# Kernel tuning notes

Measured on AMD Instinct MI355X. Metric: run time of the kernel, lower is better.

Reference implementation:

```python
import jax, jax.numpy as jnp
import numpy as np

EPS = 1e-5
BN_GAMMA = 1.0
BN_BETA = 1e-4  # per torch init: BN weight=1, bias=0.0001


def bn(h):
    # BatchNorm1d in training mode: biased batch variance
    mu = h.mean(axis=0)
    var = h.var(axis=0)
    return (h - mu) * (BN_GAMMA / jnp.sqrt(var + EPS)) + BN_BETA


def gcn_conv(h, W, b, row, col, n, edge_weight=None):
    # PyG-style GCNConv: linear -> add self loops (w=1) -> sym deg norm -> scatter-sum
    h = h @ W
    e = row.shape[0]
    ew = jnp.ones((e,), h.dtype) if edge_weight is None else edge_weight
    loop = jnp.arange(n, dtype=row.dtype)
    r = jnp.concatenate([row, loop])
    c = jnp.concatenate([col, loop])
    w = jnp.concatenate([ew, jnp.ones((n,), h.dtype)])
    deg = jax.ops.segment_sum(w, r, num_segments=n)
    dinv = jnp.where(deg > 0, jax.lax.rsqrt(deg + jnp.where(deg > 0, 0.0, 1.0)), 0.0)
    norm = dinv[r] * w * dinv[c]  # [E+N]
    msg = h[r] * norm[:, None]    # gather + per-edge scale
    out = jax.ops.segment_sum(msg, c, num_segments=n)  # scatter-aggregate
    return out + b


def readout(h, W1, b1, W2, b2):
    h = bn(h) @ W1 + b1
    h = bn(jax.nn.relu(h)) @ W2 + b2
    return jax.nn.log_softmax(h, axis=-1)


def setup_inputs() -> dict:
    key = jax.random.key(0)
    ks = jax.random.split(key, 12)
    N, E, F, H, C = 50000, 800000, 128, 128, 10
    s = 0.05
    return {
        "x": jax.random.normal(ks[0], (N, F), jnp.float32),
        "edge_index": jax.random.randint(ks[1], (2, E), 0, N, jnp.int32),
        "perm": jax.random.permutation(ks[2], N).astype(jnp.int32),
        "W_feat": jax.random.normal(ks[3], (F, H), jnp.float32) * s,
        "b_feat": jnp.zeros((H,), jnp.float32),
        "W_convs": jax.random.normal(ks[4], (3, H, H), jnp.float32) * s,
        "b_convs": jnp.zeros((3, H), jnp.float32),
        "W_ea": jax.random.normal(ks[5], (2 * H, 2), jnp.float32) * s,
        "b_ea": jnp.zeros((2,), jnp.float32),
        "W_na": jax.random.normal(ks[6], (H, 2), jnp.float32) * s,
        "b_na": jnp.zeros((2,), jnp.float32),
        "W_ctx": jax.random.normal(ks[7], (H, H), jnp.float32) * s,
        "b_ctx": jnp.zeros((H,), jnp.float32),
        "W_obj": jax.random.normal(ks[8], (H, H), jnp.float32) * s,
        "b_obj": jnp.zeros((H,), jnp.float32),
        "W_fc1": jax.random.normal(ks[9], (3, H, H), jnp.float32) * s,  # c,o,co
        "b_fc1": jnp.zeros((3, H), jnp.float32),
        "W_fc2": jax.random.normal(ks[10], (3, H, C), jnp.float32) * s,
        "b_fc2": jnp.zeros((3, C), jnp.float32),
    }


def reference(x, edge_index, perm, W_feat, b_feat, W_convs, b_convs, W_ea, b_ea,
              W_na, b_na, W_ctx, b_ctx, W_obj, b_obj, W_fc1, b_fc1, W_fc2, b_fc2):
    n = x.shape[0]
    row, col = edge_index[0], edge_index[1]
    h = bn(x)
    h = jax.nn.relu(h @ W_feat + b_feat)  # conv_feat has gfn=True -> pure linear
    for i in range(3):
        h = jax.nn.relu(gcn_conv(bn(h), W_convs[i], b_convs[i], row, col, n))
    edge_rep = jnp.concatenate([h[row], h[col]], axis=-1)  # [E, 2H]
    edge_att = jax.nn.softmax(edge_rep @ W_ea + b_ea, axis=-1)
    node_att = jax.nn.softmax(h @ W_na + b_na, axis=-1)
    xc = node_att[:, 0:1] * h
    xo = node_att[:, 1:2] * h
    xc = jax.nn.relu(gcn_conv(bn(xc), W_ctx, b_ctx, row, col, n, edge_att[:, 0]))
    xo = jax.nn.relu(gcn_conv(bn(xo), W_obj, b_obj, row, col, n, edge_att[:, 1]))
    xc_logis = readout(xc, W_fc1[0], b_fc1[0], W_fc2[0], b_fc2[0])
    xo_logis = readout(xo, W_fc1[1], b_fc1[1], W_fc2[1], b_fc2[1])
    xco_logis = readout(xc[perm] + xo, W_fc1[2], b_fc1[2], W_fc2[2], b_fc2[2])
    return (xc_logis, xo_logis, xco_logis)
```

## Files before the change

kernel.cpp:

```cpp
#include <hip/hip_runtime.h>
#include <math.h>

#define H 128
#define NCLS 10
#define EPS 1e-5f
#define BN_BETA 1e-4f
#define CS_BLOCKS 256

typedef unsigned short u16;
typedef unsigned int u32;
typedef __attribute__((ext_vector_type(8))) short short8;
typedef __attribute__((ext_vector_type(4))) float floatx4;

__device__ inline float bflo(u32 u) { union { u32 i; float f; } a; a.i = u << 16; return a.f; }
__device__ inline float bfhi(u32 u) { union { u32 i; float f; } a; a.i = u & 0xffff0000u; return a.f; }
__device__ inline u16 f2bf(float f) {
  union { float f; u32 i; } v; v.f = f;
  return (u16)((v.i + 0x7fff + ((v.i >> 16) & 1)) >> 16);
}
__device__ inline u32 pack2(float a, float b) { return (u32)f2bf(a) | ((u32)f2bf(b) << 16); }

__device__ inline void reduce_partials(const float* __restrict__ P, int nb, int stride,
                                       int off0, int f, float* su_out, float* sq_out) {
  float su[8] = {0, 0, 0, 0, 0, 0, 0, 0}, sq[8] = {0, 0, 0, 0, 0, 0, 0, 0};
  int b = 0;
  for (; b + 8 <= nb; b += 8) {
#pragma unroll
    for (int u = 0; u < 8; u++) {
      const float* p = P + (size_t)(b + u) * stride + off0;
      su[u] += p[f];
      sq[u] += p[128 + f];
    }
  }
  for (; b < nb; b++) {
    const float* p = P + (size_t)b * stride + off0;
    su[0] += p[f];
    sq[0] += p[128 + f];
  }
  *su_out = ((su[0] + su[1]) + (su[2] + su[3])) + ((su[4] + su[5]) + (su[6] + su[7]));
  *sq_out = ((sq[0] + sq[1]) + (sq[2] + sq[3])) + ((sq[4] + sq[5]) + (sq[6] + sq[7]));
}

__global__ __launch_bounds__(256) void xstats_kernel(
    const float* __restrict__ x, int n4, float* __restrict__ stp) {
  int tid = threadIdx.x;
  int lane = tid & 63, wave = tid >> 6;
  float s[4] = {0, 0, 0, 0}, q[4] = {0, 0, 0, 0};
  int step = gridDim.x * 256;
  for (int i = blockIdx.x * 256 + tid; i < n4; i += step) {
    float4 v = ((const float4*)x)[i];
    s[0] += v.x; q[0] += v.x * v.x; s[1] += v.y; q[1] += v.y * v.y;
    s[2] += v.z; q[2] += v.z * v.z; s[3] += v.w; q[3] += v.w * v.w;
  }
#pragma unroll
  for (int k = 0; k < 4; k++) { s[k] += __shfl_xor(s[k], 32); q[k] += __shfl_xor(q[k], 32); }
  __shared__ float sm[4][256];
  int col = (lane & 31) * 4;
  if (lane < 32) {
#pragma unroll
    for (int k = 0; k < 4; k++) { sm[wave][col + k] = s[k]; sm[wave][128 + col + k] = q[k]; }
  }
  __syncthreads();
  stp[(size_t)blockIdx.x * 256 + tid] = sm[0][tid] + sm[1][tid] + sm[2][tid] + sm[3][tid];
}

__global__ __launch_bounds__(256) void colstats_kernel(
    const u16* __restrict__ X, int N, float* __restrict__ stp) {
  int tid = threadIdx.x;
  int li = tid & 15, rg = tid >> 4;
  int wave = tid >> 6, lane = tid & 63;
  const uint4* T = (const uint4*)X;
  float s[8] = {0, 0, 0, 0, 0, 0, 0, 0}, q[8] = {0, 0, 0, 0, 0, 0, 0, 0};
  for (int r = blockIdx.x * 16 + rg; r < N; r += CS_BLOCKS * 16) {
    uint4 u = T[(size_t)r * 16 + li];
    float f[8] = {bflo(u.x), bfhi(u.x), bflo(u.y), bfhi(u.y),
                  bflo(u.z), bfhi(u.z), bflo(u.w), bfhi(u.w)};
#pragma unroll
    for (int j = 0; j < 8; j++) { s[j] += f[j]; q[j] += f[j] * f[j]; }
  }
#pragma unroll
  for (int j = 0; j < 8; j++) {
    s[j] += __shfl_xor(s[j], 16); s[j] += __shfl_xor(s[j], 32);
    q[j] += __shfl_xor(q[j], 16); q[j] += __shfl_xor(q[j], 32);
  }
  __shared__ float sm[4][256];
  if ((lane & 48) == 0) {
#pragma unroll
    for (int j = 0; j < 8; j++) {
      sm[wave][li * 8 + j] = s[j];
      sm[wave][128 + li * 8 + j] = q[j];
    }
  }
  __syncthreads();
  stp[(size_t)blockIdx.x * 256 + tid] = sm[0][tid] + sm[1][tid] + sm[2][tid] + sm[3][tid];
}

__device__ inline void fold_body(const float* P, int nb, int stride, int off0,
                                 const float* W, const float* bias,
                                 float invN, int k, u16* Wt, float* cf) {
  int f = threadIdx.x;
  float su, sq;
  reduce_partials(P, nb, stride, off0, f, &su, &sq);
  float mu = su * invN;
  float var = sq * invN - mu * mu;
  float s = 1.0f / sqrtf(fmaxf(var, 0.f) + EPS);
  float w = W[(size_t)f * H + k];
  Wt[(size_t)k * H + f] = f2bf(s * w);
  __shared__ float red[H];
  red[f] = (BN_BETA - mu * s) * w;
  __syncthreads();
  for (int o = 64; o > 0; o >>= 1) {
    if (f < o) red[f] += red[f + o];
    __syncthreads();
  }
  if (f == 0) cf[k] = red[0] + (bias ? bias[k] : 0.f);
}

__global__ __launch_bounds__(128) void fold_kernel(
    const float* P, int nb, const float* W, const float* bias, float invN,
    u16* Wt, float* cf) {
  fold_body(P, nb, 256, 0, W, bias, invN, blockIdx.x, Wt, cf);
}

__global__ __launch_bounds__(128) void fold2_kernel(
    const float* P, int nb, const float* W0, const float* W1, float invN,
    u16* Wt2, float* cf2) {
  int j = blockIdx.x >> 7, k = blockIdx.x & 127;
  fold_body(P, nb, 512, j * 256, j ? W1 : W0, nullptr, invN, k,
            Wt2 + (size_t)j * H * H, cf2 + j * H);
}

__global__ __launch_bounds__(128) void fold3_kernel(
    const float* PC, int nbC, const float* PO, int nbO, const float* PCO, int nbCO,
    const float* W_fc1, const float* b_fc1, float invN, u16* Wt3, float* cf3) {
  int j = blockIdx.x >> 7, k = blockIdx.x & 127;
  const float* P = (j == 0) ? PC : (j == 1) ? PO : PCO;
  int nb = (j == 0) ? nbC : (j == 1) ? nbO : nbCO;
  fold_body(P, nb, 256, 0, W_fc1 + (size_t)j * H * H, b_fc1 + j * H, invN, k,
            Wt3 + (size_t)j * H * H, cf3 + j * H);
}

__global__ __launch_bounds__(128) void fold10x3_kernel(
    const float* stpZ, int nb, const float* W_fc2, const float* b_fc2, float invN,
    float* W2f, float* c2f) {
  int j = blockIdx.x / NCLS, k = blockIdx.x % NCLS;
  const float* P = stpZ + (size_t)j * nb * 256;
  int f = threadIdx.x;
  float su, sq;
  reduce_partials(P, nb, 256, 0, f, &su, &sq);
  float mu = su * invN;
  float var = sq * invN - mu * mu;
  float s = 1.0f / sqrtf(fmaxf(var, 0.f) + EPS);
  float w = W_fc2[(size_t)j * H * NCLS + (size_t)f * NCLS + k];
  W2f[(size_t)j * H * NCLS + (size_t)f * NCLS + k] = s * w;
  __shared__ float red[H];
  red[f] = (BN_BETA - mu * s) * w;
  __syncthreads();
  for (int o = 64; o > 0; o >>= 1) {
    if (f < o) red[f] += red[f + o];
    __syncthreads();
  }
  if (f == 0) c2f[j * 16 + k] = red[0] + b_fc2[j * NCLS + k];
}

__device__ inline void gemm_core(const u16* A, const float* Afp, const u16* Bt,
                                 const float* cf, const float* b2, const float* sumw,
                                 u16* C, int N, int relu, int blk, float* stp) {
  int tid = threadIdx.x;
  int wave = tid >> 6, lane = tid & 63;
  int l15 = lane & 15, quad = lane >> 4;
  int row0 = (blk * 4 + wave) * 16;
  if (row0 >= N && !stp) return;
  int arow = row0 + l15;
  short8 a[4];
  short8 z8 = {0, 0, 0, 0, 0, 0, 0, 0};
  if (Afp) {
#pragma unroll
    for (int k4 = 0; k4 < 4; k4++) {
      if (arow < N) {
        const float* p = Afp + (size_t)arow * H + k4 * 32 + quad * 8;
        float4 f0 = *(const float4*)p;
        float4 f1 = *(const float4*)(p + 4);
        union { short8 s8; u32 u[4]; } cv;
        cv.u[0] = pack2(f0.x, f0.y); cv.u[1] = pack2(f0.z, f0.w);
        cv.u[2] = pack2(f1.x, f1.y); cv.u[3] = pack2(f1.z, f1.w);
        a[k4] = cv.s8;
      } else a[k4] = z8;
    }
  } else {
#pragma unroll
    for (int k4 = 0; k4 < 4; k4++)
      a[k4] = (arow < N) ? *(const short8*)(A + (size_t)arow * H + k4 * 32 + quad * 8) : z8;
  }
  float srow[4];
  if (sumw) {
#pragma unroll
    for (int r = 0; r < 4; r++) {
      int row = row0 + quad * 4 + r;
      srow[r] = (row < N) ? sumw[row] : 0.f;
    }
  }
  float ps[8], pq[8];
#pragma unroll
  for (int nt = 0; nt < 8; nt++) {
    floatx4 acc = {0.f, 0.f, 0.f, 0.f};
    const u16* bp = Bt + (size_t)(nt * 16 + l15) * H + quad * 8;
#pragma unroll
    for (int k4 = 0; k4 < 4; k4++) {
      short8 b = *(const short8*)(bp + k4 * 32);
      acc = __builtin_amdgcn_mfma_f32_16x16x32_bf16(a[k4], b, acc, 0, 0, 0);
    }
    int col = nt * 16 + l15;
    float base = cf[col];
    float bb = b2 ? b2[col] : 0.f;
    float s_ = 0.f, q_ = 0.f;
#pragma unroll
    for (int r = 0; r < 4; r++) {
      int row = row0 + quad * 4 + r;
      if (row < N) {
        float v = acc[r] + (sumw ? srow[r] * base + bb : base);
        if (relu) v = fmaxf(v, 0.f);
        s_ += v; q_ += v * v;
        C[(size_t)row * H + col] = f2bf(v);
      }
    }
    ps[nt] = s_; pq[nt] = q_;
  }
  if (stp) {
    __shared__ float sred[4][256];
#pragma unroll
    for (int nt = 0; nt < 8; nt++) {
      ps[nt] += __shfl_xor(ps[nt], 16); ps[nt] += __shfl_xor(ps[nt], 32);
      pq[nt] += __shfl_xor(pq[nt], 16); pq[nt] += __shfl_xor(pq[nt], 32);
    }
    if (quad == 0) {
#pragma unroll
      for (int nt = 0; nt < 8; nt++) {
        sred[wave][nt * 16 + l15] = ps[nt];
        sred[wave][128 + nt * 16 + l15] = pq[nt];
      }
    }
    __syncthreads();
    stp[(size_t)blk * 256 + tid] =
        sred[0][tid] + sred[1][tid] + sred[2][tid] + sred[3][tid];
  }
}

__global__ __launch_bounds__(256) void gemm_kernel(
    const u16* A, const u16* Bt, const float* cf, u16* C, int N, int relu) {
  gemm_core(A, nullptr, Bt, cf, nullptr, nullptr, C, N, relu, blockIdx.x, nullptr);
}

__global__ __launch_bounds__(256) void gemm_x_kernel(
    const float* x, const u16* Bt, const float* cf, u16* C, int N, float* stp) {
  gemm_core(nullptr, x, Bt, cf, nullptr, nullptr, C, N, 1, blockIdx.x, stp);
}

__global__ __launch_bounds__(256) void gemm2sw_kernel(
    u16* B0, u16* B1, const u16* Wt2, const float* cf2,
    const float* b0, const float* b1, const float* sw0, const float* sw1,
    int N, int gG, float* stp) {
  int j = blockIdx.x / gG, blk = blockIdx.x % gG;
  u16* Z = j ? B1 : B0;
  gemm_core(Z, nullptr, Wt2 + (size_t)j * H * H, cf2 + j * H, j ? b1 : b0,
            j ? sw1 : sw0, Z, N, 1, blk, stp + (size_t)j * gG * 256);
}

__global__ __launch_bounds__(256) void gemm3_kernel(
    u16* Z0, u16* Z1, u16* Z2, const u16* Wt3, const float* cf3,
    int N, int gG, float* stp) {
  int j = blockIdx.x / gG, blk = blockIdx.x % gG;
  u16* Z = (j == 0) ? Z0 : (j == 1) ? Z1 : Z2;
  gemm_core(Z, nullptr, Wt3 + (size_t)j * H * H, cf3 + j * H, nullptr, nullptr,
            Z, N, 1, blk, stp + (size_t)j * gG * 256);
}

__global__ __launch_bounds__(256) void hist_kernel(
    const int* __restrict__ row, const int* __restrict__ col, int E,
    int* __restrict__ cnt, float* __restrict__ deg) {
  int e = blockIdx.x * 256 + threadIdx.x;
  if (e < E) {
    atomicAdd(&cnt[col[e]], 1);
    atomicAdd(&deg[row[e]], 1.0f);
  }
}

__global__ __launch_bounds__(256) void scanA_rsqrt_kernel(
    const int* __restrict__ cnt, const float* __restrict__ deg, int N,
    int* __restrict__ partial, float* __restrict__ dinv) {
  int i = blockIdx.x * 256 + threadIdx.x;
  if (i < N) dinv[i] = 1.0f / sqrtf(deg[i] + 1.0f);
  __shared__ int sd[256];
  sd[threadIdx.x] = (i < N) ? cnt[i] : 0;
  __syncthreads();
  for (int o = 128; o > 0; o >>= 1) {
    if (threadIdx.x < o) sd[threadIdx.x] += sd[threadIdx.x + o];
    __syncthreads();
  }
  if (threadIdx.x == 0) partial[blockIdx.x] = sd[0];
}

__global__ __launch_bounds__(256) void scanB_kernel(const int* __restrict__ partial, int nb,
                                                    int* __restrict__ blockoff) {
  __shared__ int sd[256];
  int t = threadIdx.x;
  int v = (t < nb) ? partial[t] : 0;
  sd[t] = v;
  __syncthreads();
  for (int o = 1; o < 256; o <<= 1) {
    int x = (t >= o) ? sd[t - o] : 0;
    __syncthreads();
    sd[t] += x;
    __syncthreads();
  }
  blockoff[t] = sd[t] - v;
}

__global__ __launch_bounds__(256) void scanC_kernel(
    const int* __restrict__ cnt, int N, const int* __restrict__ blockoff,
    int* __restrict__ off, int* __restrict__ cur, int E) {
  __shared__ int sd[256];
  int t = threadIdx.x;
  int i = blockIdx.x * 256 + t;
  int v = (i < N) ? cnt[i] : 0;
  sd[t] = v;
  __syncthreads();
  for (int o = 1; o < 256; o <<= 1) {
    int x = (t >= o) ? sd[t - o] : 0;
    __syncthreads();
    sd[t] += x;
    __syncthreads();
  }
  if (i < N) {
    int ex = blockoff[blockIdx.x] + sd[t] - v;
    off[i] = ex;
    cur[i] = ex;
  }
  if (i == 0) off[N] = E;
}

__global__ __launch_bounds__(256) void place_kernel(
    const int* __restrict__ row, const int* __restrict__ col, int E,
    int* __restrict__ cur, const float* __restrict__ dinv,
    int* __restrict__ csr_src, int* __restrict__ slot_of, float* __restrict__ wn) {
  int e = blockIdx.x * 256 + threadIdx.x;
  if (e < E) {
    int r = row[e];
    int slot = atomicAdd(&cur[col[e]], 1);
    csr_src[slot] = r;
    slot_of[e] = slot;
    wn[slot] = dinv[r];
  }
}

__global__ __launch_bounds__(256) void rsqrt2_kernel(
    const float* __restrict__ deg, const float* __restrict__ degc,
    float* __restrict__ dinvc, float* __restrict__ dinvo, int N) {
  int v = blockIdx.x * 256 + threadIdx.x;
  if (v < N) {
    float dc = degc[v];
    dinvc[v] = 1.0f / sqrtf(dc + 1.0f);
    dinvo[v] = 1.0f / sqrtf(deg[v] - dc + 1.0f);
  }
}

__global__ __launch_bounds__(256) void wa2_kernel(
    const int* csr_src, float* att_and_wa0r, const float* dinvc, const float* dinvo,
    const float2* na01, float* wa0n, float* wa1n, float* wa1r, int E) {
  int i = blockIdx.x * 256 + threadIdx.x;
  if (i >= E) return;
  int s = csr_src[i];
  float a0 = att_and_wa0r[i];
  float2 na = na01[s];
  float r0 = a0 * dinvc[s];
  float r1 = (1.0f - a0) * dinvo[s];
  wa0n[i] = r0 * na.x;
  wa1n[i] = r1 * na.y;
  att_and_wa0r[i] = r0;
  wa1r[i] = r1;
}

#define ACC8(A, U, W)                                             \
  A[0] += (W) * bflo(U.x); A[1] += (W) * bfhi(U.x);               \
  A[2] += (W) * bflo(U.y); A[3] += (W) * bfhi(U.y);               \
  A[4] += (W) * bflo(U.z); A[5] += (W) * bfhi(U.z);               \
  A[6] += (W) * bflo(U.w); A[7] += (W) * bfhi(U.w);

__global__ __launch_bounds__(256) void agg_kernel(
    const u16* __restrict__ t, const int* __restrict__ csr_src,
    const float* __restrict__ wseg, const int* __restrict__ off,
    const float* __restrict__ dinv, const float* __restrict__ bias,
    u16* __restrict__ out, int N) {
  int v = blockIdx.x * 4 + (threadIdx.x >> 6);
  if (v >= N) return;
  int lane = threadIdx.x & 63;
  int g = lane >> 4, li = lane & 15;
  const uint4* T = (const uint4*)t;
  float dv = dinv[v];
  float acc[8] = {0.f, 0.f, 0.f, 0.f, 0.f, 0.f, 0.f, 0.f};
  if (g == 0) {
    uint4 u = T[(size_t)v * 16 + li];
    float w0 = dv * dv;
    ACC8(acc, u, w0)
  }
  int s0 = off[v], s1 = off[v + 1];
  for (int s = s0; s < s1; s += 32) {
    int ix[8]; float wv[8];
#pragma unroll
    for (int u = 0; u < 8; u++) {
      int e = s + g + u * 4;
      bool ok = e < s1;
      int e2 = ok ? e : s0;
      ix[u] = csr_src[e2];
      wv[u] = ok ? wseg[e2] : 0.f;
    }
    uint4 uu[8];
#pragma unroll
    for (int u = 0; u < 8; u++) uu[u] = T[(size_t)ix[u] * 16 + li];
#pragma unroll
    for (int u = 0; u < 8; u++) { float w = wv[u] * dv; ACC8(acc, uu[u], w) }
  }
#pragma unroll
  for (int j = 0; j < 8; j++) {
    acc[j] += __shfl_xor(acc[j], 16);
    acc[j] += __shfl_xor(acc[j], 32);
  }
  if (g == 0) {
    float o[8];
#pragma unroll
    for (int j = 0; j < 8; j++) o[j] = fmaxf(acc[j] + bias[li * 8 + j], 0.f);
    uint4 w4;
    w4.x = pack2(o[0], o[1]); w4.y = pack2(o[2], o[3]);
    w4.z = pack2(o[4], o[5]); w4.w = pack2(o[6], o[7]);
    ((uint4*)out)[(size_t)v * 16 + li] = w4;
  }
}

__global__ __launch_bounds__(256) void aggdual_kernel(
    const u16* __restrict__ h, const int* __restrict__ csr_src,
    const float* __restrict__ wa0n, const float* __restrict__ wa1n,
    const float* __restrict__ wa0r, const float* __restrict__ wa1r,
    const int* __restrict__ off, const float* __restrict__ dinvc,
    const float* __restrict__ dinvo, const float2* __restrict__ na01,
    u16* __restrict__ gc, u16* __restrict__ go,
    float* __restrict__ sumw_c, float* __restrict__ sumw_o, int N) {
  int v = blockIdx.x * 4 + (threadIdx.x >> 6);
  if (v >= N) return;
  int lane = threadIdx.x & 63;
  int g = lane >> 4, li = lane & 15;
  const uint4* T = (const uint4*)h;
  float dvc = dinvc[v], dvo = dinvo[v];
  float ac[8] = {0.f, 0.f, 0.f, 0.f, 0.f, 0.f, 0.f, 0.f};
  float ao[8] = {0.f, 0.f, 0.f, 0.f, 0.f, 0.f, 0.f, 0.f};
  float swc = 0.f, swo = 0.f;
  if (g == 0) {
    uint4 u = T[(size_t)v * 16 + li];
    float2 na = na01[v];
    float wc = dvc * dvc, wo = dvo * dvo;
    float wch = wc * na.x, woh = wo * na.y;
    ACC8(ac, u, wch)
    ACC8(ao, u, woh)
  }
  int s0 = off[v], s1 = off[v + 1];
  for (int s = s0; s < s1; s += 16) {
    int ix[4]; float w0n[4], w1n[4], w0r[4], w1r[4];
#pragma unroll
    for (int u = 0; u < 4; u++) {
      int e = s + g + u * 4;
      bool ok = e < s1;
      int e2 = ok ? e : s0;
      ix[u] = csr_src[e2];
      w0n[u] = ok ? wa0n[e2] : 0.f;
      w1n[u] = ok ? wa1n[e2] : 0.f;
      w0r[u] = ok ? wa0r[e2] : 0.f;
      w1r[u] = ok ? wa1r[e2] : 0.f;
    }
    uint4 uu[4];
#pragma unroll
    for (int u = 0; u < 4; u++) uu[u] = T[(size_t)ix[u] * 16 + li];
#pragma unroll
    for (int u = 0; u < 4; u++) {
      float wc = w0n[u] * dvc; ACC8(ac, uu[u], wc)
      float wo = w1n[u] * dvo; ACC8(ao, uu[u], wo)
      swc += w0r[u]; swo += w1r[u];
    }
  }
#pragma unroll
  for (int j = 0; j < 8; j++) {
    ac[j] += __shfl_xor(ac[j], 16); ac[j] += __shfl_xor(ac[j], 32);
    ao[j] += __shfl_xor(ao[j], 16); ao[j] += __shfl_xor(ao[j], 32);
  }
  swc += __shfl_xor(swc, 16); swc += __shfl_xor(swc, 32);
  swo += __shfl_xor(swo, 16); swo += __shfl_xor(swo, 32);
  if (g == 0) {
    uint4 wc4, wo4;
    wc4.x = pack2(ac[0], ac[1]); wc4.y = pack2(ac[2], ac[3]);
    wc4.z = pack2(ac[4], ac[5]); wc4.w = pack2(ac[6], ac[7]);
    wo4.x = pack2(ao[0], ao[1]); wo4.y = pack2(ao[2], ao[3]);
    wo4.z = pack2(ao[4], ao[5]); wo4.w = pack2(ao[6], ao[7]);
    ((uint4*)gc)[(size_t)v * 16 + li] = wc4;
    ((uint4*)go)[(size_t)v * 16 + li] = wo4;
    if (li == 0) {
      sumw_c[v] = dvc * swc + dvc * dvc;
      sumw_o[v] = dvo * swo + dvo * dvo;
    }
  }
}

__global__ __launch_bounds__(256) void natt_kernel(
    const u16* __restrict__ h, int N,
    const float* __restrict__ W_na, const float* __restrict__ b_na,
    const float* __restrict__ W_ea,
    float2* __restrict__ na01, float2* __restrict__ p01, float2* __restrict__ q01) {
  int n = blockIdx.x * 256 + threadIdx.x;
  if (n >= N) return;
  float sa0 = 0, sa1 = 0, sp0 = 0, sp1 = 0, sq0 = 0, sq1 = 0;
  const uint2* hr = (const uint2*)(h + (size_t)n * H);
  for (int c = 0; c < 32; c++) {
    uint2 u = hr[c];
    float v0 = bflo(u.x), v1 = bfhi(u.x), v2 = bflo(u.y), v3 = bfhi(u.y);
    int k = c * 4;
    sa0 += v0 * W_na[k * 2] + v1 * W_na[k * 2 + 2] + v2 * W_na[k * 2 + 4] + v3 * W_na[k * 2 + 6];
    sa1 += v0 * W_na[k * 2 + 1] + v1 * W_na[k * 2 + 3] + v2 * W_na[k * 2 + 5] + v3 * W_na[k * 2 + 7];
    sp0 += v0 * W_ea[k * 2] + v1 * W_ea[k * 2 + 2] + v2 * W_ea[k * 2 + 4] + v3 * W_ea[k * 2 + 6];
    sp1 += v0 * W_ea[k * 2 + 1] + v1 * W_ea[k * 2 + 3] + v2 * W_ea[k * 2 + 5] + v3 * W_ea[k * 2 + 7];
    sq0 += v0 * W_ea[(H + k) * 2] + v1 * W_ea[(H + k) * 2 + 2] + v2 * W_ea[(H + k) * 2 + 4] + v3 * W_ea[(H + k) * 2 + 6];
    sq1 += v0 * W_ea[(H + k) * 2 + 1] + v1 * W_ea[(H + k) * 2 + 3] + v2 * W_ea[(H + k) * 2 + 5] + v3 * W_ea[(H + k) * 2 + 7];
  }
  sa0 += b_na[0]; sa1 += b_na[1];
  float m = fmaxf(sa0, sa1);
  float e0 = expf(sa0 - m), e1 = expf(sa1 - m);
  float inv = 1.f / (e0 + e1);
  na01[n] = make_float2(e0 * inv, e1 * inv);
  p01[n] = make_float2(sp0, sp1);
  q01[n] = make_float2(sq0, sq1);
}

__global__ __launch_bounds__(256) void xprestats_kernel(
    const u16* __restrict__ h, const float2* __restrict__ na01, int n4,
    float* __restrict__ stp) {
  int tid = threadIdx.x;
  int lane = tid & 63, wave = tid >> 6;
  float sc[4] = {0, 0, 0, 0}, qc[4] = {0, 0, 0, 0};
  float so[4] = {0, 0, 0, 0}, qo[4] = {0, 0, 0, 0};
  int step = gridDim.x * 256;
  for (int i = blockIdx.x * 256 + tid; i < n4; i += step) {
    int n = i >> 5;
    uint2 u = ((const uint2*)h)[i];
    float v0 = bflo(u.x), v1 = bfhi(u.x), v2 = bflo(u.y), v3 = bfhi(u.y);
    float2 ab = na01[n];
    float a = ab.x, b = ab.y;
    float c0 = v0 * a, c1 = v1 * a, c2 = v2 * a, c3 = v3 * a;
    float o0 = v0 * b, o1 = v1 * b, o2 = v2 * b, o3 = v3 * b;
    sc[0] += c0; qc[0] += c0 * c0; sc[1] += c1; qc[1] += c1 * c1;
    sc[2] += c2; qc[2] += c2 * c2; sc[3] += c3; qc[3] += c3 * c3;
    so[0] += o0; qo[0] += o0 * o0; so[1] += o1; qo[1] += o1 * o1;
    so[2] += o2; qo[2] += o2 * o2; so[3] += o3; qo[3] += o3 * o3;
  }
#pragma unroll
  for (int k = 0; k < 4; k++) {
    sc[k] += __shfl_xor(sc[k], 32); qc[k] += __shfl_xor(qc[k], 32);
    so[k] += __shfl_xor(so[k], 32); qo[k] += __shfl_xor(qo[k], 32);
  }
  __shared__ float sm[4][512];
  int col = (lane & 31) * 4;
  if (lane < 32) {
#pragma unroll
    for (int k = 0; k < 4; k++) {
      sm[wave][col + k] = sc[k];
      sm[wave][128 + col + k] = qc[k];
      sm[wave][256 + col + k] = so[k];
      sm[wave][384 + col + k] = qo[k];
    }
  }
  __syncthreads();
  float r0 = sm[0][tid] + sm[1][tid] + sm[2][tid] + sm[3][tid];
  float r1 = sm[0][256 + tid] + sm[1][256 + tid] + sm[2][256 + tid] + sm[3][256 + tid];
  stp[(size_t)blockIdx.x * 512 + tid] = r0;
  stp[(size_t)blockIdx.x * 512 + 256 + tid] = r1;
}

__global__ __launch_bounds__(256) void eatt_kernel(
    const int* __restrict__ row, const int* __restrict__ col, int E,
    const float2* __restrict__ p01, const float2* __restrict__ q01,
    const float* __restrict__ b_ea, const int* __restrict__ slot_of,
    float* __restrict__ att0s, float* __restrict__ degc) {
  int e = blockIdx.x * 256 + threadIdx.x;
  if (e >= E) return;
  int r = row[e], c = col[e];
  float2 p = p01[r], q = q01[c];
  float l0 = p.x + q.x + b_ea[0];
  float l1 = p.y + q.y + b_ea[1];
  float a0 = 1.0f / (1.0f + expf(l1 - l0));
  att0s[slot_of[e]] = a0;
  atomicAdd(&degc[r], a0);
}

__global__ __launch_bounds__(256) void permadd_stats_kernel(
    const u16* __restrict__ xc, const u16* __restrict__ xo,
    const int* __restrict__ perm, u16* __restrict__ out, int n4, float* __restrict__ stp) {
  int tid = threadIdx.x;
  int lane = tid & 63, wave = tid >> 6;
  float s[4] = {0, 0, 0, 0}, q[4] = {0, 0, 0, 0};
  int step = gridDim.x * 256;
  for (int i = blockIdx.x * 256 + tid; i < n4; i += step) {
    int n = i >> 5, k = i & 31;
    int p = perm[n];
    uint2 a = ((const uint2*)xc)[(size_t)p * 32 + k];
    uint2 b = ((const uint2*)xo)[i];
    float f0 = bflo(a.x) + bflo(b.x), f1 = bfhi(a.x) + bfhi(b.x);
    float f2 = bflo(a.y) + bflo(b.y), f3 = bfhi(a.y) + bfhi(b.y);
    ((uint2*)out)[i] = make_uint2(pack2(f0, f1), pack2(f2, f3));
    s[0] += f0; q[0] += f0 * f0; s[1] += f1; q[1] += f1 * f1;
    s[2] += f2; q[2] += f2 * f2; s[3] += f3; q[3] += f3 * f3;
  }
#pragma unroll
  for (int k = 0; k < 4; k++) { s[k] += __shfl_xor(s[k], 32); q[k] += __shfl_xor(q[k], 32); }
  __shared__ float sm[4][256];
  int col = (lane & 31) * 4;
  if (lane < 32) {
#pragma unroll
    for (int k = 0; k < 4; k++) { sm[wave][col + k] = s[k]; sm[wave][128 + col + k] = q[k]; }
  }
  __syncthreads();
  stp[(size_t)blockIdx.x * 256 + tid] = sm[0][tid] + sm[1][tid] + sm[2][tid] + sm[3][tid];
}

__global__ __launch_bounds__(256) void fc2x3_kernel(
    const u16* __restrict__ z0, const u16* __restrict__ z1, const u16* __restrict__ z2,
    const float* __restrict__ W2f, const float* __restrict__ c2f,
    float* __restrict__ outp, int N, int gN) {
  int j = blockIdx.x / gN, blk = blockIdx.x % gN;
  int n = blk * 256 + threadIdx.x;
  if (n >= N) return;
  const u16* z = (j == 0) ? z0 : (j == 1) ? z1 : z2;
  const float* W2 = W2f + (size_t)j * H * NCLS;
  const float* c2 = c2f + j * 16;
  float* op = outp + (size_t)j * N * NCLS;
  float acc[NCLS];
#pragma unroll
  for (int c = 0; c < NCLS; c++) acc[c] = c2[c];
  const uint2* zr = (const uint2*)(z + (size_t)n * H);
  for (int c4 = 0; c4 < 32; c4++) {
    uint2 u = zr[c4];
    float v[4] = {bflo(u.x), bfhi(u.x), bflo(u.y), bfhi(u.y)};
    int k = c4 * 4;
#pragma unroll
    for (int jj = 0; jj < 4; jj++)
#pragma unroll
      for (int c = 0; c < NCLS; c++) acc[c] += v[jj] * W2[(k + jj) * NCLS + c];
  }
  float m = acc[0];
#pragma unroll
  for (int c = 1; c < NCLS; c++) m = fmaxf(m, acc[c]);
  float s = 0.f;
#pragma unroll
  for (int c = 0; c < NCLS; c++) s += expf(acc[c] - m);
  float lse = logf(s) + m;
#pragma unroll
  for (int c = 0; c < NCLS; c++) op[(size_t)n * NCLS + c] = acc[c] - lse;
}

extern "C" void kernel_launch(void* const* d_in, const int* in_sizes, int n_in,
                              void* d_out, int out_size, void* d_ws, size_t ws_size,
                              hipStream_t stream) {
  const int N = in_sizes[0] / H;
  const int E = in_sizes[1] / 2;
  const float* x = (const float*)d_in[0];
  const int* ei = (const int*)d_in[1];
  const int* row = ei;
  const int* col = ei + E;
  const int* perm = (const int*)d_in[2];
  const float* W_feat = (const float*)d_in[3];
  const float* b_feat = (const float*)d_in[4];
  const float* W_convs = (const float*)d_in[5];
  const float* b_convs = (const float*)d_in[6];
  const float* W_ea = (const float*)d_in[7];
  const float* b_ea = (const float*)d_in[8];
  const float* W_na = (const float*)d_in[9];
  const float* b_na = (const float*)d_in[10];
  const float* W_ctx = (const float*)d_in[11];
  const float* b_ctx = (const float*)d_in[12];
  const float* W_obj = (const float*)d_in[13];
  const float* b_obj = (const float*)d_in[14];
  const float* W_fc1 = (const float*)d_in[15];
  const float* b_fc1 = (const float*)d_in[16];
  const float* W_fc2 = (const float*)d_in[17];
  const float* b_fc2 = (const float*)d_in[18];
  float* out = (float*)d_out;

  const int gG = (N + 63) / 64;
  const int gN = (N + 255) / 256;
  const int gE = (E + 255) / 256;
  const int SB = (N + 255) / 256;
  const int n4 = N * 32;
  const int gAgg = (N + 3) / 4;
  const float invN = 1.0f / (float)N;

  char* base = (char*)d_ws;
  size_t off_b = 0;
  auto alloc = [&](size_t bytes) -> void* {
    void* p = base + off_b;
    off_b = (off_b + bytes + 255) & ~(size_t)255;
    return p;
  };
  size_t NB2 = (size_t)N * H * sizeof(u16);
  u16* bufA = (u16*)alloc(NB2);
  u16* bufB = (u16*)alloc(NB2);
  u16* bufC = (u16*)alloc(NB2);
  u16* bufD = (u16*)alloc(NB2);
  int* cnt = (int*)alloc(3 * (size_t)N * 4);
  float* deg = (float*)(cnt + N);
  float* degc = (float*)(cnt + 2 * (size_t)N);
  float* stpX = (float*)alloc((size_t)CS_BLOCKS * 256 * 4);
  float* stpG = (float*)alloc(3 * (size_t)gG * 256 * 4);
  float* stpPre = (float*)alloc((size_t)CS_BLOCKS * 512 * 4);
  float* stpCO = (float*)alloc((size_t)CS_BLOCKS * 256 * 4);
  int* off = (int*)alloc(((size_t)N + 1) * 4);
  int* cur = (int*)alloc((size_t)N * 4);
  float* dinv = (float*)alloc((size_t)N * 4);
  float* dinvc = (float*)alloc((size_t)N * 4);
  float* dinvo = (float*)alloc((size_t)N * 4);
  float* sumw_c = (float*)alloc((size_t)N * 4);
  float* sumw_o = (float*)alloc((size_t)N * 4);
  float2* na01 = (float2*)alloc((size_t)N * 8);
  float2* p01 = (float2*)alloc((size_t)N * 8);
  float2* q01 = (float2*)alloc((size_t)N * 8);
  int* partial = (int*)alloc(256 * 4);
  int* blockoff = (int*)alloc(256 * 4);
  u16* Wt = (u16*)alloc((size_t)H * H * 2);
  u16* Wt2 = (u16*)alloc(2 * (size_t)H * H * 2);
  u16* Wt3 = (u16*)alloc(3 * (size_t)H * H * 2);
  float* cf = (float*)alloc(H * 4);
  float* cf2 = (float*)alloc(2 * H * 4);
  float* cf3 = (float*)alloc(3 * H * 4);
  float* W2f = (float*)alloc(3 * (size_t)H * NCLS * 4);
  float* c2f = (float*)alloc(3 * 16 * 4);
  int* csr_src = (int*)alloc((size_t)E * 4);
  int* slot_of = (int*)alloc((size_t)E * 4);
  float* att0s = (float*)alloc((size_t)E * 4);
  float* wn = (float*)alloc((size_t)E * 4);
  float* waX = (float*)alloc((size_t)E * 4);
  float* wa0n = (float*)slot_of;
  float* wa1n = wn;
  float* wa0r = att0s;
  float* wa1r = waX;

  hipMemsetAsync(cnt, 0, 3 * (size_t)N * 4, stream);

  hist_kernel<<<gE, 256, 0, stream>>>(row, col, E, cnt, deg);
  scanA_rsqrt_kernel<<<SB, 256, 0, stream>>>(cnt, deg, N, partial, dinv);
  scanB_kernel<<<1, 256, 0, stream>>>(partial, SB, blockoff);
  scanC_kernel<<<SB, 256, 0, stream>>>(cnt, N, blockoff, off, cur, E);
  place_kernel<<<gE, 256, 0, stream>>>(row, col, E, cur, dinv, csr_src, slot_of, wn);

  xstats_kernel<<<CS_BLOCKS, 256, 0, stream>>>(x, n4, stpX);
  fold_kernel<<<H, H, 0, stream>>>(stpX, CS_BLOCKS, W_feat, b_feat, invN, Wt, cf);
  gemm_x_kernel<<<gG, 256, 0, stream>>>(x, Wt, cf, bufA, N, stpG);

  const float* stprev = stpG;
  int nbprev = gG;
  for (int i = 0; i < 3; ++i) {
    fold_kernel<<<H, H, 0, stream>>>(stprev, nbprev, W_convs + (size_t)i * H * H,
                                     nullptr, invN, Wt, cf);
    gemm_kernel<<<gG, 256, 0, stream>>>(bufA, Wt, cf, bufB, N, 0);
    agg_kernel<<<gAgg, 256, 0, stream>>>(bufB, csr_src, wn, off, dinv,
                                         b_convs + (size_t)i * H, bufA, N);
    if (i < 2) {
      colstats_kernel<<<CS_BLOCKS, 256, 0, stream>>>(bufA, N, stpX);
      stprev = stpX; nbprev = CS_BLOCKS;
    }
  }

  natt_kernel<<<gN, 256, 0, stream>>>(bufA, N, W_na, b_na, W_ea, na01, p01, q01);
  eatt_kernel<<<gE, 256, 0, stream>>>(row, col, E, p01, q01, b_ea, slot_of, att0s, degc);
  rsqrt2_kernel<<<gN, 256, 0, stream>>>(deg, degc, dinvc, dinvo, N);
  wa2_kernel<<<gE, 256, 0, stream>>>(csr_src, att0s, dinvc, dinvo, na01,
                                     wa0n, wa1n, wa1r, E);
  xprestats_kernel<<<CS_BLOCKS, 256, 0, stream>>>(bufA, na01, n4, stpPre);

  fold2_kernel<<<2 * H, H, 0, stream>>>(stpPre, CS_BLOCKS, W_ctx, W_obj, invN, Wt2, cf2);
  aggdual_kernel<<<gAgg, 256, 0, stream>>>(bufA, csr_src, wa0n, wa1n, wa0r, wa1r,
                                           off, dinvc, dinvo, na01, bufC, bufD,
                                           sumw_c, sumw_o, N);
  gemm2sw_kernel<<<2 * gG, 256, 0, stream>>>(bufC, bufD, Wt2, cf2, b_ctx, b_obj,
                                             sumw_c, sumw_o, N, gG, stpG);

  permadd_stats_kernel<<<CS_BLOCKS, 256, 0, stream>>>(bufC, bufD, perm, bufA, n4, stpCO);

  fold3_kernel<<<3 * H, H, 0, stream>>>(stpG, gG, stpG + (size_t)gG * 256, gG,
                                        stpCO, CS_BLOCKS, W_fc1, b_fc1, invN, Wt3, cf3);
  gemm3_kernel<<<3 * gG, 256, 0, stream>>>(bufC, bufD, bufA, Wt3, cf3, N, gG, stpG);
  fold10x3_kernel<<<3 * NCLS, H, 0, stream>>>(stpG, gG, W_fc2, b_fc2, invN, W2f, c2f);
  fc2x3_kernel<<<3 * gN, 256, 0, stream>>>(bufC, bufD, bufA, W2f, c2f, out, N, gN);
}
```

Baseline: 920.0 us.

## Aggregate before GEMM in GCN layers and fuse bias, ReLU, stats into GEMM

Reorders each of the three GCN layers to aggregate the normalized input first, then run the GEMM with a per-node sumw term that carries the BN shift and bias. ReLU and column statistics move into the GEMM epilogue, which removes the separate colstats pass and the extra elementwise epilogue in aggregation. The per-edge attention weights are also packed into two float2 arrays, so the dual aggregation issues fewer scattered loads. The cost is new buffers and more reliance on the gemm_core epilogue being correct for this case. Aggregating before the transform also reorders bf16 rounding.

```diff
diff --git a/kernel.cpp b/kernel.cpp
--- a/kernel.cpp
+++ b/kernel.cpp
@@ -59,37 +59,6 @@
   if (lane < 32) {
 #pragma unroll
     for (int k = 0; k < 4; k++) { sm[wave][col + k] = s[k]; sm[wave][128 + col + k] = q[k]; }
-  }
-  __syncthreads();
-  stp[(size_t)blockIdx.x * 256 + tid] = sm[0][tid] + sm[1][tid] + sm[2][tid] + sm[3][tid];
-}
-
-__global__ __launch_bounds__(256) void colstats_kernel(
-    const u16* __restrict__ X, int N, float* __restrict__ stp) {
-  int tid = threadIdx.x;
-  int li = tid & 15, rg = tid >> 4;
-  int wave = tid >> 6, lane = tid & 63;
-  const uint4* T = (const uint4*)X;
-  float s[8] = {0, 0, 0, 0, 0, 0, 0, 0}, q[8] = {0, 0, 0, 0, 0, 0, 0, 0};
-  for (int r = blockIdx.x * 16 + rg; r < N; r += CS_BLOCKS * 16) {
-    uint4 u = T[(size_t)r * 16 + li];
-    float f[8] = {bflo(u.x), bfhi(u.x), bflo(u.y), bfhi(u.y),
-                  bflo(u.z), bfhi(u.z), bflo(u.w), bfhi(u.w)};
-#pragma unroll
-    for (int j = 0; j < 8; j++) { s[j] += f[j]; q[j] += f[j] * f[j]; }
-  }
-#pragma unroll
-  for (int j = 0; j < 8; j++) {
-    s[j] += __shfl_xor(s[j], 16); s[j] += __shfl_xor(s[j], 32);
-    q[j] += __shfl_xor(q[j], 16); q[j] += __shfl_xor(q[j], 32);
-  }
-  __shared__ float sm[4][256];
-  if ((lane & 48) == 0) {
-#pragma unroll
-    for (int j = 0; j < 8; j++) {
-      sm[wave][li * 8 + j] = s[j];
-      sm[wave][128 + li * 8 + j] = q[j];
-    }
   }
   __syncthreads();
   stp[(size_t)blockIdx.x * 256 + tid] = sm[0][tid] + sm[1][tid] + sm[2][tid] + sm[3][tid];
@@ -246,14 +215,15 @@
   }
 }
 
-__global__ __launch_bounds__(256) void gemm_kernel(
-    const u16* A, const u16* Bt, const float* cf, u16* C, int N, int relu) {
-  gemm_core(A, nullptr, Bt, cf, nullptr, nullptr, C, N, relu, blockIdx.x, nullptr);
-}
-
 __global__ __launch_bounds__(256) void gemm_x_kernel(
     const float* x, const u16* Bt, const float* cf, u16* C, int N, float* stp) {
   gemm_core(nullptr, x, Bt, cf, nullptr, nullptr, C, N, 1, blockIdx.x, stp);
+}
+
+__global__ __launch_bounds__(256) void gemmsw_kernel(
+    const u16* G, const u16* Wt, const float* cf, const float* b2,
+    const float* sumw, u16* C, int N, float* stp) {
+  gemm_core(G, nullptr, Wt, cf, b2, sumw, C, N, 1, blockIdx.x, stp);
 }
 
 __global__ __launch_bounds__(256) void gemm2sw_kernel(
@@ -365,19 +335,17 @@
 }
 
 __global__ __launch_bounds__(256) void wa2_kernel(
-    const int* csr_src, float* att_and_wa0r, const float* dinvc, const float* dinvo,
-    const float2* na01, float* wa0n, float* wa1n, float* wa1r, int E) {
+    const int* csr_src, const float* att0s, const float* dinvc, const float* dinvo,
+    const float2* na01, float2* wfa, float2* wfr, int E) {
   int i = blockIdx.x * 256 + threadIdx.x;
   if (i >= E) return;
   int s = csr_src[i];
-  float a0 = att_and_wa0r[i];
+  float a0 = att0s[i];
   float2 na = na01[s];
   float r0 = a0 * dinvc[s];
   float r1 = (1.0f - a0) * dinvo[s];
-  wa0n[i] = r0 * na.x;
-  wa1n[i] = r1 * na.y;
-  att_and_wa0r[i] = r0;
-  wa1r[i] = r1;
+  wfa[i] = make_float2(r0 * na.x, r1 * na.y);
+  wfr[i] = make_float2(r0, r1);
 }
 
 #define ACC8(A, U, W)                                             \
@@ -386,18 +354,19 @@
   A[4] += (W) * bflo(U.z); A[5] += (W) * bfhi(U.z);               \
   A[6] += (W) * bflo(U.w); A[7] += (W) * bfhi(U.w);
 
-__global__ __launch_bounds__(256) void agg_kernel(
-    const u16* __restrict__ t, const int* __restrict__ csr_src,
-    const float* __restrict__ wseg, const int* __restrict__ off,
-    const float* __restrict__ dinv, const float* __restrict__ bias,
-    u16* __restrict__ out, int N) {
+__global__ __launch_bounds__(256) void aggn_kernel(
+    const u16* __restrict__ h, const int* __restrict__ csr_src,
+    const float* __restrict__ wn, const int* __restrict__ off,
+    const float* __restrict__ dinv, u16* __restrict__ gout,
+    float* __restrict__ sumw, int N) {
   int v = blockIdx.x * 4 + (threadIdx.x >> 6);
   if (v >= N) return;
   int lane = threadIdx.x & 63;
   int g = lane >> 4, li = lane & 15;
-  const uint4* T = (const uint4*)t;
+  const uint4* T = (const uint4*)h;
   float dv = dinv[v];
   float acc[8] = {0.f, 0.f, 0.f, 0.f, 0.f, 0.f, 0.f, 0.f};
+  float sw = 0.f;
   if (g == 0) {
     uint4 u = T[(size_t)v * 16 + li];
     float w0 = dv * dv;
@@ -412,34 +381,32 @@
       bool ok = e < s1;
       int e2 = ok ? e : s0;
       ix[u] = csr_src[e2];
-      wv[u] = ok ? wseg[e2] : 0.f;
+      wv[u] = ok ? wn[e2] : 0.f;
     }
     uint4 uu[8];
 #pragma unroll
     for (int u = 0; u < 8; u++) uu[u] = T[(size_t)ix[u] * 16 + li];
 #pragma unroll
-    for (int u = 0; u < 8; u++) { float w = wv[u] * dv; ACC8(acc, uu[u], w) }
+    for (int u = 0; u < 8; u++) { float w = wv[u] * dv; ACC8(acc, uu[u], w) sw += wv[u]; }
   }
 #pragma unroll
   for (int j = 0; j < 8; j++) {
     acc[j] += __shfl_xor(acc[j], 16);
     acc[j] += __shfl_xor(acc[j], 32);
   }
+  sw += __shfl_xor(sw, 16); sw += __shfl_xor(sw, 32);
   if (g == 0) {
-    float o[8];
-#pragma unroll
-    for (int j = 0; j < 8; j++) o[j] = fmaxf(acc[j] + bias[li * 8 + j], 0.f);
     uint4 w4;
-    w4.x = pack2(o[0], o[1]); w4.y = pack2(o[2], o[3]);
-    w4.z = pack2(o[4], o[5]); w4.w = pack2(o[6], o[7]);
-    ((uint4*)out)[(size_t)v * 16 + li] = w4;
+    w4.x = pack2(acc[0], acc[1]); w4.y = pack2(acc[2], acc[3]);
+    w4.z = pack2(acc[4], acc[5]); w4.w = pack2(acc[6], acc[7]);
+    ((uint4*)gout)[(size_t)v * 16 + li] = w4;
+    if (sumw && li == 0) sumw[v] = dv * sw + dv * dv;
   }
 }
 
 __global__ __launch_bounds__(256) void aggdual_kernel(
     const u16* __restrict__ h, const int* __restrict__ csr_src,
-    const float* __restrict__ wa0n, const float* __restrict__ wa1n,
-    const float* __restrict__ wa0r, const float* __restrict__ wa1r,
+    const float2* __restrict__ wfa, const float2* __restrict__ wfr,
     const int* __restrict__ off, const float* __restrict__ dinvc,
     const float* __restrict__ dinvo, const float2* __restrict__ na01,
     u16* __restrict__ gc, u16* __restrict__ go,
@@ -463,26 +430,24 @@
   }
   int s0 = off[v], s1 = off[v + 1];
   for (int s = s0; s < s1; s += 16) {
-    int ix[4]; float w0n[4], w1n[4], w0r[4], w1r[4];
+    int ix[4]; float2 fa[4], fr[4];
 #pragma unroll
     for (int u = 0; u < 4; u++) {
       int e = s + g + u * 4;
       bool ok = e < s1;
       int e2 = ok ? e : s0;
       ix[u] = csr_src[e2];
-      w0n[u] = ok ? wa0n[e2] : 0.f;
-      w1n[u] = ok ? wa1n[e2] : 0.f;
-      w0r[u] = ok ? wa0r[e2] : 0.f;
-      w1r[u] = ok ? wa1r[e2] : 0.f;
+      fa[u] = ok ? wfa[e2] : make_float2(0.f, 0.f);
+      fr[u] = ok ? wfr[e2] : make_float2(0.f, 0.f);
     }
     uint4 uu[4];
 #pragma unroll
     for (int u = 0; u < 4; u++) uu[u] = T[(size_t)ix[u] * 16 + li];
 #pragma unroll
     for (int u = 0; u < 4; u++) {
-      float wc = w0n[u] * dvc; ACC8(ac, uu[u], wc)
-      float wo = w1n[u] * dvo; ACC8(ao, uu[u], wo)
-      swc += w0r[u]; swo += w1r[u];
+      float wc = fa[u].x * dvc; ACC8(ac, uu[u], wc)
+      float wo = fa[u].y * dvo; ACC8(ao, uu[u], wo)
+      swc += fr[u].x; swo += fr[u].y;
     }
   }
 #pragma unroll
@@ -721,6 +686,7 @@
   float* dinv = (float*)alloc((size_t)N * 4);
   float* dinvc = (float*)alloc((size_t)N * 4);
   float* dinvo = (float*)alloc((size_t)N * 4);
+  float* sumw_n = (float*)alloc((size_t)N * 4);
   float* sumw_c = (float*)alloc((size_t)N * 4);
   float* sumw_o = (float*)alloc((size_t)N * 4);
   float2* na01 = (float2*)alloc((size_t)N * 8);
@@ -740,11 +706,8 @@
   int* slot_of = (int*)alloc((size_t)E * 4);
   float* att0s = (float*)alloc((size_t)E * 4);
   float* wn = (float*)alloc((size_t)E * 4);
-  float* waX = (float*)alloc((size_t)E * 4);
-  float* wa0n = (float*)slot_of;
-  float* wa1n = wn;
-  float* wa0r = att0s;
-  float* wa1r = waX;
+  float2* wfa = (float2*)alloc((size_t)E * 8);
+  float2* wfr = (float2*)alloc((size_t)E * 8);
 
   hipMemsetAsync(cnt, 0, 3 * (size_t)N * 4, stream);
 
@@ -758,31 +721,24 @@
   fold_kernel<<<H, H, 0, stream>>>(stpX, CS_BLOCKS, W_feat, b_feat, invN, Wt, cf);
   gemm_x_kernel<<<gG, 256, 0, stream>>>(x, Wt, cf, bufA, N, stpG);
 
-  const float* stprev = stpG;
-  int nbprev = gG;
   for (int i = 0; i < 3; ++i) {
-    fold_kernel<<<H, H, 0, stream>>>(stprev, nbprev, W_convs + (size_t)i * H * H,
+    fold_kernel<<<H, H, 0, stream>>>(stpG, gG, W_convs + (size_t)i * H * H,
                                      nullptr, invN, Wt, cf);
-    gemm_kernel<<<gG, 256, 0, stream>>>(bufA, Wt, cf, bufB, N, 0);
-    agg_kernel<<<gAgg, 256, 0, stream>>>(bufB, csr_src, wn, off, dinv,
-                                         b_convs + (size_t)i * H, bufA, N);
-    if (i < 2) {
-      colstats_kernel<<<CS_BLOCKS, 256, 0, stream>>>(bufA, N, stpX);
-      stprev = stpX; nbprev = CS_BLOCKS;
-    }
+    aggn_kernel<<<gAgg, 256, 0, stream>>>(bufA, csr_src, wn, off, dinv, bufB,
+                                          (i == 0) ? sumw_n : nullptr, N);
+    gemmsw_kernel<<<gG, 256, 0, stream>>>(bufB, Wt, cf, b_convs + (size_t)i * H,
+                                          sumw_n, bufA, N, stpG);
   }
 
   natt_kernel<<<gN, 256, 0, stream>>>(bufA, N, W_na, b_na, W_ea, na01, p01, q01);
   eatt_kernel<<<gE, 256, 0, stream>>>(row, col, E, p01, q01, b_ea, slot_of, att0s, degc);
   rsqrt2_kernel<<<gN, 256, 0, stream>>>(deg, degc, dinvc, dinvo, N);
-  wa2_kernel<<<gE, 256, 0, stream>>>(csr_src, att0s, dinvc, dinvo, na01,
-                                     wa0n, wa1n, wa1r, E);
+  wa2_kernel<<<gE, 256, 0, stream>>>(csr_src, att0s, dinvc, dinvo, na01, wfa, wfr, E);
   xprestats_kernel<<<CS_BLOCKS, 256, 0, stream>>>(bufA, na01, n4, stpPre);
 
   fold2_kernel<<<2 * H, H, 0, stream>>>(stpPre, CS_BLOCKS, W_ctx, W_obj, invN, Wt2, cf2);
-  aggdual_kernel<<<gAgg, 256, 0, stream>>>(bufA, csr_src, wa0n, wa1n, wa0r, wa1r,
-                                           off, dinvc, dinvo, na01, bufC, bufD,
-                                           sumw_c, sumw_o, N);
+  aggdual_kernel<<<gAgg, 256, 0, stream>>>(bufA, csr_src, wfa, wfr, off, dinvc,
+                                           dinvo, na01, bufC, bufD, sumw_c, sumw_o, N);
   gemm2sw_kernel<<<2 * gG, 256, 0, stream>>>(bufC, bufD, Wt2, cf2, b_ctx, b_obj,
                                              sumw_c, sumw_o, N, gG, stpG);
 
```

Result: slower. 970.0 us (+5.4%).
